# Kernel optimization log

Measured on AMD Instinct MI355X. Metric: run time of the kernel, lower is better.

The kernel has to match this reference:

```python
import jax, jax.numpy as jnp
import numpy as np

DIM = 768
NUM_HEADS = 12
HEAD_DIM = DIM // NUM_HEADS
EPS = 1e-5


def setup_inputs() -> dict:
    key = jax.random.key(0)
    ks = jax.random.split(key, 6)
    s = 1.0 / np.sqrt(DIM)
    return {
        "x": jax.random.normal(ks[0], (8, 1024, DIM), dtype=jnp.float32),
        "qkv_w": jax.random.uniform(ks[1], (3 * DIM, DIM), jnp.float32, -s, s),
        "qkv_b": jax.random.uniform(ks[2], (3 * DIM,), jnp.float32, -s, s),
        "proj_w": jax.random.uniform(ks[3], (DIM, DIM), jnp.float32, -s, s),
        "proj_b": jax.random.uniform(ks[4], (DIM,), jnp.float32, -s, s),
        "qn_gamma": jnp.ones((HEAD_DIM,), jnp.float32),
        "qn_beta": jnp.zeros((HEAD_DIM,), jnp.float32),
    }


def _layernorm(x, gamma, beta):
    mu = jnp.mean(x, axis=-1, keepdims=True)
    var = jnp.var(x, axis=-1, keepdims=True)
    return (x - mu) * jax.lax.rsqrt(var + EPS) * gamma + beta


def reference(x, qkv_w, qkv_b, proj_w, proj_b, qn_gamma, qn_beta):
    B, N, D = x.shape
    scale = HEAD_DIM ** -0.5
    qkv = x @ qkv_w.T + qkv_b  # [B, N, 3*D]
    qkv = qkv.reshape(B, N, 3, NUM_HEADS, HEAD_DIM).transpose(2, 0, 3, 1, 4)
    q, k, v = qkv[0], qkv[1], qkv[2]  # each [B, H, N, hd]
    # Original code applies q_norm to BOTH q and k (faithful to source).
    q = _layernorm(q, qn_gamma, qn_beta)
    k = _layernorm(k, qn_gamma, qn_beta)
    scores = jnp.einsum("bhqd,bhkd->bhqk", q, k) * scale  # [B, H, N, N]
    attn = jax.nn.softmax(scores, axis=-1)
    out = jnp.einsum("bhqk,bhkd->bhqd", attn, v)  # [B, H, N, hd]
    out = out.transpose(0, 2, 1, 3).reshape(B, N, D)
    return out @ proj_w.T + proj_b
```

## Files before the change

kernel.cpp:

```cpp
#include <hip/hip_runtime.h>
#include <stdint.h>

#define DIM   768
#define NHEAD 12
#define HD    64
#define BATCH 8
#define SEQ   1024
#define MROWS (BATCH * SEQ)
#define EPSLN 1e-5f
#define QK_SCALE (0.125f * 1.44269504f)

typedef __attribute__((ext_vector_type(8))) short s8v;
typedef __attribute__((ext_vector_type(4))) short s4v;
typedef __attribute__((ext_vector_type(4))) float f32x4;

__device__ inline short f2bf(float f) {
    union { float f; unsigned u; } v; v.f = f;
    unsigned r = v.u + 0x7FFFu + ((v.u >> 16) & 1u);
    return (short)(r >> 16);
}
__device__ inline unsigned pk2bf(float lo, float hi) {
    union { float f; unsigned u; } a, b; a.f = lo; b.f = hi;
    return __builtin_amdgcn_perm(b.u + 0x8000u, a.u + 0x8000u, 0x07060302u);
}
__device__ inline void gload16(const void* g, void* l) {
    __builtin_amdgcn_global_load_lds(
        (const __attribute__((address_space(1))) void*)g,
        (__attribute__((address_space(3))) void*)l, 16, 0, 0);
}

#define N4_X (MROWS * DIM / 4)
#define N4_W1 (3 * DIM * DIM / 4)
#define N4_W2 (DIM * DIM / 4)
__global__ __launch_bounds__(256) void cvt_all(
    const float* __restrict__ x, const float* __restrict__ w1,
    const float* __restrict__ w2, short* __restrict__ dx,
    short* __restrict__ dw1, short* __restrict__ dw2)
{
    size_t i = (size_t)blockIdx.x * 256 + threadIdx.x;
    const float* s; short* d;
    if (i < N4_X)                { s = x  + i * 4;               d = dx  + i * 4; }
    else if (i < N4_X + N4_W1)   { size_t j = i - N4_X;          s = w1 + j * 4; d = dw1 + j * 4; }
    else                         { size_t j = i - N4_X - N4_W1;  s = w2 + j * 4; d = dw2 + j * 4; }
    float4 v = *(const float4*)s;
    uint2 o; o.x = pk2bf(v.x, v.y); o.y = pk2bf(v.z, v.w);
    *(uint2*)d = o;
}

template<int BM>
__global__ __launch_bounds__(256) void gemm_mfma(
    const short* __restrict__ A, const short* __restrict__ W,
    const float* __restrict__ bias,
    short* __restrict__ oq, short* __restrict__ ok, short* __restrict__ ov,
    float* __restrict__ oplain, int Ncols, int qkv_mode,
    const float* __restrict__ gamma, const float* __restrict__ beta)
{
    constexpr int MT = BM / 32;
    __shared__ __align__(16) short As[2][BM * 64];
    __shared__ __align__(16) short Bs[2][128 * 64];

    const int tid  = threadIdx.x;
    const int gx    = gridDim.x;
    const int id    = blockIdx.y * gx + blockIdx.x;
    const int chunk = (gx * gridDim.y) >> 3;
    const int vid   = (id & 7) * chunk + (id >> 3);
    const int m0   = (vid / gx) * BM;
    const int n0   = (vid % gx) * 128;
    const int w    = tid >> 6, lane = tid & 63;
    const int quad = lane >> 4, l16 = lane & 15;
    const int wm   = (w & 1) * (BM / 2), wn = (w >> 1) * 64;
    const int rsw  = l16 & 7;

    f32x4 acc[MT][4];
#pragma unroll
    for (int i = 0; i < MT; ++i)
#pragma unroll
        for (int j = 0; j < 4; ++j) acc[i][j] = (f32x4){0.f, 0.f, 0.f, 0.f};

    auto stage = [&](int buf, int k0) {
#pragma unroll
        for (int i = 0; i < BM / 32; ++i) {
            int f   = i * 256 + tid;
            int row = f >> 3;
            int c   = (f & 7) ^ (row & 7);
            gload16(&A[(size_t)(m0 + row) * DIM + k0 + c * 8], &As[buf][f * 8]);
        }
#pragma unroll
        for (int i = 0; i < 4; ++i) {
            int f   = i * 256 + tid;
            int row = f >> 3;
            int c   = (f & 7) ^ (row & 7);
            gload16(&W[(size_t)(n0 + row) * DIM + k0 + c * 8], &Bs[buf][f * 8]);
        }
    };

    constexpr int NK = DIM / 64;
    stage(0, 0);
    __syncthreads();

    for (int t = 0; t < NK; ++t) {
        const int cur = t & 1;
        if (t + 1 < NK) stage(cur ^ 1, (t + 1) * 64);
#pragma unroll
        for (int ks = 0; ks < 2; ++ks) {
            const int ch = ((ks * 4 + quad) ^ rsw) * 8;
            s8v af[MT], bw[4];
#pragma unroll
            for (int t2 = 0; t2 < MT; ++t2)
                af[t2] = *(const s8v*)&As[cur][(wm + t2 * 16 + l16) * 64 + ch];
#pragma unroll
            for (int t2 = 0; t2 < 4; ++t2)
                bw[t2] = *(const s8v*)&Bs[cur][(wn + t2 * 16 + l16) * 64 + ch];
#pragma unroll
            for (int mt = 0; mt < MT; ++mt)
#pragma unroll
                for (int nt = 0; nt < 4; ++nt)
                    acc[mt][nt] = __builtin_amdgcn_mfma_f32_16x16x32_bf16(
                        af[mt], bw[nt], acc[mt][nt], 0, 0, 0);
        }
        __syncthreads();
    }

    if (qkv_mode) {
        const int which = n0 / DIM;
        if (which == 2) {
#pragma unroll
            for (int mt = 0; mt < MT; ++mt)
#pragma unroll
                for (int nt = 0; nt < 4; ++nt)
#pragma unroll
                    for (int i = 0; i < 4; ++i) {
                        int m  = m0 + wm + mt * 16 + quad * 4 + i;
                        int n  = n0 + wn + nt * 16 + l16;
                        float cv = acc[mt][nt][i] + bias[n];
                        int bb = m >> 10, nn = m & 1023;
                        int d  = n - 2 * DIM;
                        int hh = d >> 6, e = d & 63;
                        ov[(((size_t)(bb * NHEAD + hh)) * HD + e) * SEQ + nn] = f2bf(cv);
                    }
        } else {
            const float qs = (which == 0) ? QK_SCALE : 1.0f;
            short* dst = which ? ok : oq;
            const int hh = (n0 + wn - which * DIM) >> 6;
            float ge[4], be[4];
#pragma unroll
            for (int nt = 0; nt < 4; ++nt) {
                ge[nt] = gamma[nt * 16 + l16];
                be[nt] = beta [nt * 16 + l16] * qs;
            }
#pragma unroll
            for (int mt = 0; mt < MT; ++mt)
#pragma unroll
                for (int i = 0; i < 4; ++i) {
                    float cv[4], s = 0.f, s2 = 0.f;
#pragma unroll
                    for (int nt = 0; nt < 4; ++nt) {
                        int n = n0 + wn + nt * 16 + l16;
                        cv[nt] = acc[mt][nt][i] + bias[n];
                        s  += cv[nt];
                        s2 += cv[nt] * cv[nt];
                    }
                    s  += __shfl_xor(s, 1);  s  += __shfl_xor(s, 2);
                    s  += __shfl_xor(s, 4);  s  += __shfl_xor(s, 8);
                    s2 += __shfl_xor(s2, 1); s2 += __shfl_xor(s2, 2);
                    s2 += __shfl_xor(s2, 4); s2 += __shfl_xor(s2, 8);
                    float mu  = s * (1.f / 64.f);
                    float var = s2 * (1.f / 64.f) - mu * mu;
                    float rs  = rsqrtf(var + EPSLN) * qs;
                    int m  = m0 + wm + mt * 16 + quad * 4 + i;
                    int bb = m >> 10, nn = m & 1023;
                    short* rp = &dst[(((size_t)(bb * NHEAD + hh)) * SEQ + nn) * HD];
#pragma unroll
                    for (int nt = 0; nt < 4; ++nt) {
                        float val = (cv[nt] - mu) * rs * ge[nt] + be[nt];
                        rp[nt * 16 + l16] = f2bf(val);
                    }
                }
        }
    } else {
#pragma unroll
        for (int mt = 0; mt < MT; ++mt)
#pragma unroll
            for (int nt = 0; nt < 4; ++nt)
#pragma unroll
                for (int i = 0; i < 4; ++i) {
                    int m = m0 + wm + mt * 16 + quad * 4 + i;
                    int n = n0 + wn + nt * 16 + l16;
                    oplain[(size_t)m * Ncols + n] = acc[mt][nt][i] + bias[n];
                }
    }
}

__global__ __launch_bounds__(256) void attn_mfma(
    const short* __restrict__ q, const short* __restrict__ k,
    const short* __restrict__ vt, short* __restrict__ O)
{
    const int id   = blockIdx.y * gridDim.x + blockIdx.x;
    const int vid  = (id & 7) * 192 + (id >> 3);
    const int bh   = vid >> 4;
    const int q0   = (vid & 15) * 64;
    const int b    = bh / NHEAD;
    const int h    = bh % NHEAD;
    const int tid  = threadIdx.x;
    const int w    = tid >> 6;
    const int lane = tid & 63;
    const int quad = lane >> 4;
    const int l16  = lane & 15;

    __shared__ __align__(16) char smem[20480];
    __shared__ float denom[4][64];

    short (*Pw)[40]   = (short(*)[40])(smem + (size_t)w * (64 * 40 * 2));
    float (*Obuf)[68] = (float(*)[68])smem;

    const size_t base   = (size_t)bh * SEQ * HD;
    const size_t vtbase = (size_t)bh * HD * SEQ;

    s8v qB[4][2];
#pragma unroll
    for (int qt = 0; qt < 4; ++qt)
#pragma unroll
        for (int hf = 0; hf < 2; ++hf)
            qB[qt][hf] = *(const s8v*)&q[base + (size_t)(q0 + qt * 16 + l16) * HD
                                         + hf * 32 + quad * 8];

    f32x4 oacc[4][4];
    float lacc[4] = {0.f, 0.f, 0.f, 0.f};
#pragma unroll
    for (int a = 0; a < 4; ++a)
#pragma unroll
        for (int c = 0; c < 4; ++c) oacc[a][c] = (f32x4){0.f, 0.f, 0.f, 0.f};

#pragma unroll 2
    for (int jb = 0; jb < 8; ++jb) {
        const int kb = jb * 128 + w * 32;

        s8v kA[2][2];
#pragma unroll
        for (int kt = 0; kt < 2; ++kt)
#pragma unroll
            for (int hf = 0; hf < 2; ++hf)
                kA[kt][hf] = *(const s8v*)&k[base + (size_t)(kb + kt * 16 + l16) * HD
                                             + hf * 32 + quad * 8];
        s8v va[4];
#pragma unroll
        for (int et = 0; et < 4; ++et)
            va[et] = *(const s8v*)&vt[vtbase + (size_t)(et * 16 + l16) * SEQ
                                      + kb + quad * 8];

#pragma unroll
        for (int qt = 0; qt < 4; ++qt)
#pragma unroll
            for (int kt = 0; kt < 2; ++kt) {
                f32x4 c = (f32x4){0.f, 0.f, 0.f, 0.f};
                c = __builtin_amdgcn_mfma_f32_16x16x32_bf16(kA[kt][0], qB[qt][0], c, 0, 0, 0);
                c = __builtin_amdgcn_mfma_f32_16x16x32_bf16(kA[kt][1], qB[qt][1], c, 0, 0, 0);
                float p0 = exp2f(c[0]), p1 = exp2f(c[1]);
                float p2 = exp2f(c[2]), p3 = exp2f(c[3]);
                lacc[qt] += (p0 + p1) + (p2 + p3);
                uint2 pk; pk.x = pk2bf(p0, p1); pk.y = pk2bf(p2, p3);
                *(uint2*)&Pw[qt * 16 + l16][kt * 16 + quad * 4] = pk;
            }

        s8v pb[4];
#pragma unroll
        for (int qt = 0; qt < 4; ++qt)
            pb[qt] = *(const s8v*)&Pw[qt * 16 + l16][quad * 8];

        __builtin_amdgcn_s_setprio(1);
#pragma unroll
        for (int et = 0; et < 4; ++et)
#pragma unroll
            for (int qt = 0; qt < 4; ++qt)
                oacc[et][qt] = __builtin_amdgcn_mfma_f32_16x16x32_bf16(
                    va[et], pb[qt], oacc[et][qt], 0, 0, 0);
        __builtin_amdgcn_s_setprio(0);
    }

#pragma unroll
    for (int qt = 0; qt < 4; ++qt) {
        float s = lacc[qt];
        s += __shfl_xor(s, 16);
        s += __shfl_xor(s, 32);
        denom[w][qt * 16 + l16] = s;
    }
    __syncthreads();

    for (int r = 0; r < 4; ++r) {
        if (w == r) {
#pragma unroll
            for (int et = 0; et < 4; ++et)
#pragma unroll
                for (int qt = 0; qt < 4; ++qt) {
                    float* dst = &Obuf[qt * 16 + l16][et * 16 + quad * 4];
                    float4 ov;
                    if (r == 0) ov = make_float4(0.f, 0.f, 0.f, 0.f);
                    else        ov = *(float4*)dst;
                    ov.x += oacc[et][qt][0]; ov.y += oacc[et][qt][1];
                    ov.z += oacc[et][qt][2]; ov.w += oacc[et][qt][3];
                    *(float4*)dst = ov;
                }
        }
        __syncthreads();
    }

    const int qq = tid >> 2;
    const int e0 = (tid & 3) * 16;
    float linv = 1.0f / (denom[0][qq] + denom[1][qq] + denom[2][qq] + denom[3][qq]);
    float4 f0 = *(float4*)&Obuf[qq][e0];
    float4 f1 = *(float4*)&Obuf[qq][e0 + 4];
    float4 f2 = *(float4*)&Obuf[qq][e0 + 8];
    float4 f3 = *(float4*)&Obuf[qq][e0 + 12];
    short* op = &O[((size_t)b * SEQ + q0 + qq) * DIM + h * HD + e0];
    uint4 o1, o2;
    o1.x = pk2bf(f0.x * linv, f0.y * linv);
    o1.y = pk2bf(f0.z * linv, f0.w * linv);
    o1.z = pk2bf(f1.x * linv, f1.y * linv);
    o1.w = pk2bf(f1.z * linv, f1.w * linv);
    o2.x = pk2bf(f2.x * linv, f2.y * linv);
    o2.y = pk2bf(f2.z * linv, f2.w * linv);
    o2.z = pk2bf(f3.x * linv, f3.y * linv);
    o2.w = pk2bf(f3.z * linv, f3.w * linv);
    *(uint4*)&op[0] = o1;
    *(uint4*)&op[8] = o2;
}

extern "C" void kernel_launch(void* const* d_in, const int* in_sizes, int n_in,
                              void* d_out, int out_size, void* d_ws, size_t ws_size,
                              hipStream_t stream)
{
    const float* x      = (const float*)d_in[0];
    const float* qkv_w  = (const float*)d_in[1];
    const float* qkv_b  = (const float*)d_in[2];
    const float* proj_w = (const float*)d_in[3];
    const float* proj_b = (const float*)d_in[4];
    const float* gamma  = (const float*)d_in[5];
    const float* beta   = (const float*)d_in[6];
    float* out = (float*)d_out;

    const size_t PER = (size_t)BATCH * NHEAD * SEQ * HD;
    short* qb  = (short*)d_ws;
    short* kb  = qb + PER;
    short* vtb = kb + PER;
    short* ob  = vtb + PER;
    short* xb  = ob + PER;
    short* wqb = xb + (size_t)MROWS * DIM;
    short* wpb = wqb + (size_t)3 * DIM * DIM;

    cvt_all<<<dim3((N4_X + N4_W1 + N4_W2) / 256), 256, 0, stream>>>(
        x, qkv_w, proj_w, xb, wqb, wpb);

    gemm_mfma<128><<<dim3(2304 / 128, MROWS / 128), 256, 0, stream>>>(
        xb, wqb, qkv_b, qb, kb, vtb, nullptr, 2304, 1, gamma, beta);

    attn_mfma<<<dim3(SEQ / 64, BATCH * NHEAD), 256, 0, stream>>>(
        qb, kb, vtb, ob);

    gemm_mfma<64><<<dim3(DIM / 128, MROWS / 64), 256, 0, stream>>>(
        ob, wpb, proj_b, nullptr, nullptr, nullptr, out, DIM, 0, nullptr, nullptr);
}
```

Measured before the change: 214.1 us.

## Store Q/K/V in MFMA fragment-tiled layout and relax GEMM barriers

The QKV GEMM epilogue now writes Q, K and V in a fragment-major tiled layout, so each attention wave loads a whole MFMA operand fragment with one contiguous 512-element read (lane*8) instead of strided row gathers. V is packed four values at a time into uint2 stores. The GEMM main loop replaces __syncthreads with explicit vmcnt waits plus s_barrier so the next tile's loads can stay in flight, and the grid swizzle for block order is removed. The attention P scratch row stride goes from 40 to 44 and the jb loop unroll pragma is dropped. The risks are scattered 2-byte stores in the Q/K epilogue, weaker L2 locality without the swizzle, and hand-counted vmcnt values that must match the number of loads issued by stage().

Result: faster. 201.8 us (-5.7%).

```diff
diff --git a/kernel.cpp b/kernel.cpp
--- a/kernel.cpp
+++ b/kernel.cpp
@@ -60,12 +60,8 @@
     __shared__ __align__(16) short Bs[2][128 * 64];
 
     const int tid  = threadIdx.x;
-    const int gx    = gridDim.x;
-    const int id    = blockIdx.y * gx + blockIdx.x;
-    const int chunk = (gx * gridDim.y) >> 3;
-    const int vid   = (id & 7) * chunk + (id >> 3);
-    const int m0   = (vid / gx) * BM;
-    const int n0   = (vid % gx) * 128;
+    const int m0   = blockIdx.y * BM;
+    const int n0   = blockIdx.x * 128;
     const int w    = tid >> 6, lane = tid & 63;
     const int quad = lane >> 4, l16 = lane & 15;
     const int wm   = (w & 1) * (BM / 2), wn = (w >> 1) * 64;
@@ -96,11 +92,19 @@
 
     constexpr int NK = DIM / 64;
     stage(0, 0);
-    __syncthreads();
 
     for (int t = 0; t < NK; ++t) {
         const int cur = t & 1;
-        if (t + 1 < NK) stage(cur ^ 1, (t + 1) * 64);
+        if (t + 1 < NK) {
+            stage(cur ^ 1, (t + 1) * 64);
+            if constexpr (BM == 128)
+                asm volatile("s_waitcnt vmcnt(8)" ::: "memory");
+            else
+                asm volatile("s_waitcnt vmcnt(6)" ::: "memory");
+        } else {
+            asm volatile("s_waitcnt vmcnt(0)" ::: "memory");
+        }
+        __builtin_amdgcn_s_barrier();
 #pragma unroll
         for (int ks = 0; ks < 2; ++ks) {
             const int ch = ((ks * 4 + quad) ^ rsw) * 8;
@@ -118,35 +122,41 @@
                     acc[mt][nt] = __builtin_amdgcn_mfma_f32_16x16x32_bf16(
                         af[mt], bw[nt], acc[mt][nt], 0, 0, 0);
         }
-        __syncthreads();
+        __builtin_amdgcn_s_barrier();
     }
 
     if (qkv_mode) {
         const int which = n0 / DIM;
         if (which == 2) {
+            const int hh = (n0 + wn - 2 * DIM) >> 6;
 #pragma unroll
             for (int mt = 0; mt < MT; ++mt)
 #pragma unroll
-                for (int nt = 0; nt < 4; ++nt)
-#pragma unroll
-                    for (int i = 0; i < 4; ++i) {
-                        int m  = m0 + wm + mt * 16 + quad * 4 + i;
-                        int n  = n0 + wn + nt * 16 + l16;
-                        float cv = acc[mt][nt][i] + bias[n];
-                        int bb = m >> 10, nn = m & 1023;
-                        int d  = n - 2 * DIM;
-                        int hh = d >> 6, e = d & 63;
-                        ov[(((size_t)(bb * NHEAD + hh)) * HD + e) * SEQ + nn] = f2bf(cv);
-                    }
+                for (int nt = 0; nt < 4; ++nt) {
+                    int m  = m0 + wm + mt * 16 + quad * 4;
+                    int n  = n0 + wn + nt * 16 + l16;
+                    float c0 = acc[mt][nt][0] + bias[n];
+                    float c1 = acc[mt][nt][1] + bias[n];
+                    float c2 = acc[mt][nt][2] + bias[n];
+                    float c3 = acc[mt][nt][3] + bias[n];
+                    int bb = m >> 10, nn = m & 1023;
+                    int bh = bb * NHEAD + hh;
+                    size_t addr = ((((size_t)bh * 32 + (nn >> 5)) * 4 + nt) << 9)
+                                + (((nn & 31) >> 3) * 16 + l16) * 8 + (nn & 7);
+                    uint2 pk; pk.x = pk2bf(c0, c1); pk.y = pk2bf(c2, c3);
+                    *(uint2*)&ov[addr] = pk;
+                }
         } else {
             const float qs = (which == 0) ? QK_SCALE : 1.0f;
             short* dst = which ? ok : oq;
             const int hh = (n0 + wn - which * DIM) >> 6;
             float ge[4], be[4];
+            int suboff[4];
 #pragma unroll
             for (int nt = 0; nt < 4; ++nt) {
                 ge[nt] = gamma[nt * 16 + l16];
                 be[nt] = beta [nt * 16 + l16] * qs;
+                suboff[nt] = (nt >> 1) * 512 + ((nt & 1) * 2 + (l16 >> 3)) * 128 + (l16 & 7);
             }
 #pragma unroll
             for (int mt = 0; mt < MT; ++mt)
@@ -169,11 +179,13 @@
                     float rs  = rsqrtf(var + EPSLN) * qs;
                     int m  = m0 + wm + mt * 16 + quad * 4 + i;
                     int bb = m >> 10, nn = m & 1023;
-                    short* rp = &dst[(((size_t)(bb * NHEAD + hh)) * SEQ + nn) * HD];
+                    int bh = bb * NHEAD + hh;
+                    size_t rb = ((((size_t)bh * 32 + (nn >> 5)) * 4
+                                  + ((nn >> 4) & 1) * 2) << 9) + (nn & 15) * 8;
 #pragma unroll
                     for (int nt = 0; nt < 4; ++nt) {
                         float val = (cv[nt] - mu) * rs * ge[nt] + be[nt];
-                        rp[nt * 16 + l16] = f2bf(val);
+                        dst[rb + suboff[nt]] = f2bf(val);
                     }
                 }
         }
@@ -207,22 +219,19 @@
     const int quad = lane >> 4;
     const int l16  = lane & 15;
 
-    __shared__ __align__(16) char smem[20480];
+    __shared__ __align__(16) char smem[22528];
     __shared__ float denom[4][64];
 
-    short (*Pw)[40]   = (short(*)[40])(smem + (size_t)w * (64 * 40 * 2));
+    short (*Pw)[44]   = (short(*)[44])(smem + (size_t)w * (64 * 44 * 2));
     float (*Obuf)[68] = (float(*)[68])smem;
 
-    const size_t base   = (size_t)bh * SEQ * HD;
-    const size_t vtbase = (size_t)bh * HD * SEQ;
-
+    const size_t qg2 = ((size_t)bh * 64 + (q0 >> 4)) * 2;
     s8v qB[4][2];
 #pragma unroll
     for (int qt = 0; qt < 4; ++qt)
 #pragma unroll
         for (int hf = 0; hf < 2; ++hf)
-            qB[qt][hf] = *(const s8v*)&q[base + (size_t)(q0 + qt * 16 + l16) * HD
-                                         + hf * 32 + quad * 8];
+            qB[qt][hf] = *(const s8v*)&q[((qg2 + qt * 2 + hf) << 9) + lane * 8];
 
     f32x4 oacc[4][4];
     float lacc[4] = {0.f, 0.f, 0.f, 0.f};
@@ -231,22 +240,20 @@
 #pragma unroll
         for (int c = 0; c < 4; ++c) oacc[a][c] = (f32x4){0.f, 0.f, 0.f, 0.f};
 
-#pragma unroll 2
     for (int jb = 0; jb < 8; ++jb) {
-        const int kb = jb * 128 + w * 32;
-
+        const int kw = jb * 4 + w;
+        const size_t kb9 = (((size_t)bh * 32 + kw) * 4) << 9;
+
+        s8v va[4];
+#pragma unroll
+        for (int et = 0; et < 4; ++et)
+            va[et] = *(const s8v*)&vt[kb9 + ((size_t)et << 9) + lane * 8];
         s8v kA[2][2];
 #pragma unroll
         for (int kt = 0; kt < 2; ++kt)
 #pragma unroll
             for (int hf = 0; hf < 2; ++hf)
-                kA[kt][hf] = *(const s8v*)&k[base + (size_t)(kb + kt * 16 + l16) * HD
-                                             + hf * 32 + quad * 8];
-        s8v va[4];
-#pragma unroll
-        for (int et = 0; et < 4; ++et)
-            va[et] = *(const s8v*)&vt[vtbase + (size_t)(et * 16 + l16) * SEQ
-                                      + kb + quad * 8];
+                kA[kt][hf] = *(const s8v*)&k[kb9 + ((size_t)(kt * 2 + hf) << 9) + lane * 8];
 
 #pragma unroll
         for (int qt = 0; qt < 4; ++qt)
```
